# Performance work log

Measured on AMD Instinct MI355X. Metric: run time of the kernel, lower is better.

Reference implementation:

```python
import jax, jax.numpy as jnp
import numpy as np

B, H, S, D = 2, 16, 2048, 128
EPS = 1e-12  # F.normalize default eps
NEG = -1000000000.0


def setup_inputs() -> dict:
    key = jax.random.key(0)
    kq, kk, kv, km = jax.random.split(key, 4)
    q = jax.random.normal(kq, (B, H, S, D), dtype=jnp.float32)
    k = jax.random.normal(kk, (B, H, S, D), dtype=jnp.float32)
    v = jax.random.normal(kv, (B, H, S, D), dtype=jnp.float32)
    mask = jax.random.randint(km, (B, 1, 1, S), 0, 2).astype(jnp.int32)
    return {"q": q, "k": k, "v": v, "mask": mask}


def reference(q, k, v, mask):
    # L2-normalize k along dim=1 (the HEAD axis), matching F.normalize(k, p=2, dim=1)
    k_norm = k / jnp.maximum(jnp.linalg.norm(k, axis=1, keepdims=True), EPS)
    # attn scores: [B,H,S,S]
    attn = jnp.einsum('bhqd,bhkd->bhqk', q, k_norm)
    attn = jnp.where(mask == 0, NEG, attn)
    attn = jax.nn.softmax(attn, axis=-1)
    # dropout is identity in eval mode (deterministic reference)
    out = jnp.einsum('bhqk,bhkd->bhqd', attn, v)
    return (out, attn)
```

## Files before the change

kernel.cpp:

```cpp
#include <hip/hip_runtime.h>
#include <hip/hip_fp16.h>

#define BB 2
#define HH 16
#define SS 2048
#define DD 128
#define CH 64
#define NCH 32
#define QBLK 32
#define CSHIFT 14.0f

typedef __attribute__((ext_vector_type(8))) _Float16 f16x8;
typedef __attribute__((ext_vector_type(4))) _Float16 f16x4;
typedef __attribute__((ext_vector_type(4))) float    f32x4;

__device__ __forceinline__ void load_lds16(const void* g, void* l) {
  __builtin_amdgcn_global_load_lds(
      (const __attribute__((address_space(1))) void*)g,
      (__attribute__((address_space(3))) void*)l, 16, 0, 0);
}

__device__ __forceinline__ void block_barrier() {
  asm volatile("" ::: "memory");
  __builtin_amdgcn_s_barrier();
  asm volatile("" ::: "memory");
}

__global__ void knorm_f16(const float* __restrict__ k, _Float16* __restrict__ kh) {
  int t = blockIdx.x * 256 + threadIdx.x;
  int d = t & (DD - 1);
  int s = (t >> 7) & (SS - 1);
  int b = t >> 18;
  const float* kp = k + (size_t)b * HH * SS * DD + (size_t)s * DD + d;
  float vals[HH];
  float ss = 0.f;
  #pragma unroll
  for (int h = 0; h < HH; ++h) { float x = kp[(size_t)h * SS * DD]; vals[h] = x; ss += x * x; }
  float r = 1.0f / fmaxf(sqrtf(ss), 1e-12f);
  const int doff = (((d >> 3) ^ (s & 7)) << 3) + (d & 7);
  _Float16* op = kh + (size_t)b * HH * SS * DD + (size_t)s * DD + doff;
  #pragma unroll
  for (int h = 0; h < HH; ++h) op[(size_t)h * SS * DD] = (_Float16)(vals[h] * r);
}

__global__ void cvt_f16(const float* __restrict__ x, _Float16* __restrict__ y) {
  size_t i = ((size_t)blockIdx.x * 256 + threadIdx.x) * 8;
  float4 a = *(const float4*)(x + i);
  float4 b = *(const float4*)(x + i + 4);
  f16x8 r = { (_Float16)a.x, (_Float16)a.y, (_Float16)a.z, (_Float16)a.w,
              (_Float16)b.x, (_Float16)b.y, (_Float16)b.z, (_Float16)b.w };
  *(f16x8*)(y + i) = r;
}

__global__ void vtrans_f16(const float* __restrict__ v, _Float16* __restrict__ vt) {
  __shared__ float tile[32][33];
  int bh = blockIdx.z;
  int d0 = blockIdx.x * 32, s0 = blockIdx.y * 32;
  const float* vp = v + (size_t)bh * SS * DD;
  _Float16* tp = vt + (size_t)bh * SS * DD;
  int tx = threadIdx.x, ty = threadIdx.y;
  #pragma unroll
  for (int i = ty; i < 32; i += 8)
    tile[i][tx] = vp[(size_t)(s0 + i) * DD + d0 + tx];
  __syncthreads();
  #pragma unroll
  for (int i = ty; i < 32; i += 8) {
    const int key = s0 + tx, dd = d0 + i;
    tp[(size_t)(key >> 6) * (DD * CH) + (size_t)dd * CH
       + ((((key & 63) >> 3) ^ (dd & 7)) << 3) + (key & 7)] = (_Float16)tile[tx][i];
  }
}

__global__ __launch_bounds__(512, 4) void attn_fused(
    const _Float16* __restrict__ qh, const _Float16* __restrict__ kh,
    const _Float16* __restrict__ vth, const int* __restrict__ mask,
    float* __restrict__ out, float* __restrict__ attn)
{
  __shared__ _Float16 kbuf[2][CH * DD];
  __shared__ _Float16 vbuf[2][DD * CH];
  __shared__ _Float16 pbuf[2][QBLK * CH];
  __shared__ float redsum[2][16][5];

  const int wgid = blockIdx.x;
  const int xcd  = wgid & 7;
  const int idx  = wgid >> 3;
  const int bh   = (xcd << 2) | (idx >> 6);
  const int q0   = (idx & 63) * QBLK;
  const int b    = bh >> 4;

  const int tid  = threadIdx.x;
  const int lane = tid & 63;
  const int w    = tid >> 6;
  const int lo16 = lane & 15;
  const int g    = lane >> 4;
  const int qhf  = w >> 2;
  const int sub  = w & 3;

  const size_t hoff = (size_t)bh * SS * DD;
  const _Float16* Q = qh  + hoff + (size_t)q0 * DD;
  const _Float16* K = kh  + hoff;
  const _Float16* V = vth + hoff;
  const int* mrow = mask + b * SS;

  const int prow = qhf * 16 + lo16;

  f16x8 qf[4];
  #pragma unroll
  for (int c = 0; c < 4; ++c)
    qf[c] = *(const f16x8*)(Q + (size_t)prow * DD + c * 32 + g * 8);

  #pragma unroll
  for (int j = 0; j < 2; ++j) {
    const int slot = tid + j * 512;
    load_lds16(K + slot * 8, &kbuf[0][slot * 8]);
  }
  __syncthreads();

  f16x4 acc_h[NCH];
  f32x4 oacc[2] = { {0,0,0,0}, {0,0,0,0} };
  float ssum = 0.f;

  #pragma unroll
  for (int c = 0; c < NCH; ++c) {
    const _Float16* kb = kbuf[c & 1];

    if (c + 1 < NCH) {
      #pragma unroll
      for (int j = 0; j < 2; ++j) {
        const int slot = tid + j * 512;
        load_lds16(K + (size_t)(c + 1) * (CH * DD) + slot * 8,
                   &kbuf[(c + 1) & 1][slot * 8]);
      }
    }
    #pragma unroll
    for (int j = 0; j < 2; ++j) {
      const int slot = tid + j * 512;
      load_lds16(V + (size_t)c * (CH * DD) + slot * 8,
                 &vbuf[c & 1][slot * 8]);
    }

    {
      const int row = sub * 16 + lo16;
      f32x4 a = {0.f, 0.f, 0.f, 0.f};
      #pragma unroll
      for (int cc = 0; cc < 4; ++cc) {
        const int p = (cc * 4 + g) ^ (row & 7);
        f16x8 kf = *(const f16x8*)(kb + row * DD + p * 8);
        a = __builtin_amdgcn_mfma_f32_16x16x32_f16(kf, qf[cc], a, 0, 0, 0);
      }
      const int4 mv = *(const int4*)(mrow + c * CH + sub * 16 + g * 4);
      const float e0 = mv.x ? __expf(a[0] - CSHIFT) : 0.f;
      const float e1 = mv.y ? __expf(a[1] - CSHIFT) : 0.f;
      const float e2 = mv.z ? __expf(a[2] - CSHIFT) : 0.f;
      const float e3 = mv.w ? __expf(a[3] - CSHIFT) : 0.f;
      ssum += e0 + e1 + e2 + e3;
      f16x4 eh = { (_Float16)e0, (_Float16)e1, (_Float16)e2, (_Float16)e3 };
      acc_h[c] = eh;
      const int col = sub * 16 + g * 4;
      *(f16x4*)(&pbuf[c & 1][prow * CH + (((col >> 3) ^ (prow & 7)) << 3) + (col & 7)]) = eh;
    }

    if (c > 0) {
      const _Float16* vb = vbuf[(c - 1) & 1];
      const _Float16* pb = pbuf[(c - 1) & 1];
      #pragma unroll
      for (int t = 0; t < 2; ++t) {
        const int dcol = sub * 32 + t * 16 + lo16;
        #pragma unroll
        for (int ks = 0; ks < 2; ++ks) {
          const int pv_ = (ks * 4 + g) ^ (dcol & 7);
          f16x8 vf = *(const f16x8*)(vb + dcol * CH + pv_ * 8);
          f16x8 pf = *(const f16x8*)(pb + prow * CH + ((ks * 32 + g * 8) ^ ((prow & 7) << 3)));
          oacc[t] = __builtin_amdgcn_mfma_f32_16x16x32_f16(pf, vf, oacc[t], 0, 0, 0);
        }
      }
    }

    asm volatile("s_waitcnt lgkmcnt(0)" ::: "memory");
    asm volatile("s_waitcnt vmcnt(0)"  ::: "memory");
    block_barrier();
  }

  {
    const _Float16* vb = vbuf[(NCH - 1) & 1];
    const _Float16* pb = pbuf[(NCH - 1) & 1];
    #pragma unroll
    for (int t = 0; t < 2; ++t) {
      const int dcol = sub * 32 + t * 16 + lo16;
      #pragma unroll
      for (int ks = 0; ks < 2; ++ks) {
        const int pv_ = (ks * 4 + g) ^ (dcol & 7);
        f16x8 vf = *(const f16x8*)(vb + dcol * CH + pv_ * 8);
        f16x8 pf = *(const f16x8*)(pb + prow * CH + ((ks * 32 + g * 8) ^ ((prow & 7) << 3)));
        oacc[t] = __builtin_amdgcn_mfma_f32_16x16x32_f16(pf, vf, oacc[t], 0, 0, 0);
      }
    }
  }

  ssum += __shfl_xor(ssum, 16);
  ssum += __shfl_xor(ssum, 32);
  if (lane < 16) redsum[qhf][lane][sub] = ssum;
  __syncthreads();

  float denom = 0.f;
  #pragma unroll
  for (int j = 0; j < 4; ++j) denom += redsum[qhf][lo16][j];
  const float inv = 1.0f / denom;

  float* arow = attn + ((size_t)bh * SS + q0 + prow) * SS + sub * 16 + g * 4;
  #pragma unroll
  for (int c = 0; c < NCH; ++c) {
    f32x4 pst = { (float)acc_h[c][0] * inv, (float)acc_h[c][1] * inv,
                  (float)acc_h[c][2] * inv, (float)acc_h[c][3] * inv };
    *(f32x4*)(arow + c * CH) = pst;
  }

  float* O = out + hoff + (size_t)q0 * DD + sub * 32;
  #pragma unroll
  for (int i = 0; i < 4; ++i) {
    const int qr = g * 4 + i;
    float dq = 0.f;
    #pragma unroll
    for (int j = 0; j < 4; ++j) dq += redsum[qhf][qr][j];
    const float rdq = 1.0f / dq;
    #pragma unroll
    for (int t = 0; t < 2; ++t)
      O[(size_t)(qhf * 16 + qr) * DD + t * 16 + lo16] = oacc[t][i] * rdq;
  }
}

extern "C" void kernel_launch(void* const* d_in, const int* in_sizes, int n_in,
                              void* d_out, int out_size, void* d_ws, size_t ws_size,
                              hipStream_t stream) {
  const float* q    = (const float*)d_in[0];
  const float* k    = (const float*)d_in[1];
  const float* v    = (const float*)d_in[2];
  const int*   mask = (const int*)d_in[3];

  const size_t N = (size_t)BB * HH * SS * DD;
  float* out  = (float*)d_out;
  float* attn = out + N;

  _Float16* qh  = (_Float16*)d_ws;
  _Float16* kh  = qh + N;
  _Float16* vth = kh + N;

  cvt_f16  <<<N / 8 / 256, 256, 0, stream>>>(q, qh);
  knorm_f16<<<(BB * SS * DD) / 256, 256, 0, stream>>>(k, kh);
  vtrans_f16<<<dim3(DD / 32, SS / 32, BB * HH), dim3(32, 8), 0, stream>>>(v, vth);

  attn_fused<<<2048, 512, 0, stream>>>(qh, kh, vth, mask, out, attn);
}
```

Measured before the change: 313.1 us.

## Double query block per workgroup and triple-buffer K/V prefetch two chunks ahead

Each workgroup now handles 64 query rows with 1024 threads (16 waves), so every K/V chunk loaded into LDS is shared by twice as many rows and the grid is halved. K and V use triple buffering: K is prefetched two chunks ahead and V one chunk ahead, and the per-iteration wait becomes vmcnt(1), which lets the most recent K load stay in flight across the barrier. The larger workgroup raises LDS use, and the 1024-thread launch bounds may cap registers per thread, which could cause spills given the large per-thread array of f16 score fragments.

Result: no change. 316.4 us (+1.0%).

```diff
diff --git a/kernel.cpp b/kernel.cpp
--- a/kernel.cpp
+++ b/kernel.cpp
@@ -7,7 +7,7 @@
 #define DD 128
 #define CH 64
 #define NCH 32
-#define QBLK 32
+#define QBLK 64
 #define CSHIFT 14.0f
 
 typedef __attribute__((ext_vector_type(8))) _Float16 f16x8;
@@ -71,21 +71,21 @@
   }
 }
 
-__global__ __launch_bounds__(512, 4) void attn_fused(
+__global__ __launch_bounds__(1024, 4) void attn_fused(
     const _Float16* __restrict__ qh, const _Float16* __restrict__ kh,
     const _Float16* __restrict__ vth, const int* __restrict__ mask,
     float* __restrict__ out, float* __restrict__ attn)
 {
-  __shared__ _Float16 kbuf[2][CH * DD];
-  __shared__ _Float16 vbuf[2][DD * CH];
+  __shared__ _Float16 kbuf[3][CH * DD];
+  __shared__ _Float16 vbuf[3][DD * CH];
   __shared__ _Float16 pbuf[2][QBLK * CH];
-  __shared__ float redsum[2][16][5];
+  __shared__ float redsum[4][16][5];
 
   const int wgid = blockIdx.x;
   const int xcd  = wgid & 7;
   const int idx  = wgid >> 3;
-  const int bh   = (xcd << 2) | (idx >> 6);
-  const int q0   = (idx & 63) * QBLK;
+  const int bh   = (xcd << 2) | (idx >> 5);
+  const int q0   = (idx & 31) * QBLK;
   const int b    = bh >> 4;
 
   const int tid  = threadIdx.x;
@@ -93,7 +93,7 @@
   const int w    = tid >> 6;
   const int lo16 = lane & 15;
   const int g    = lane >> 4;
-  const int qhf  = w >> 2;
+  const int qq   = w >> 2;
   const int sub  = w & 3;
 
   const size_t hoff = (size_t)bh * SS * DD;
@@ -102,18 +102,16 @@
   const _Float16* V = vth + hoff;
   const int* mrow = mask + b * SS;
 
-  const int prow = qhf * 16 + lo16;
+  const int prow = qq * 16 + lo16;
 
   f16x8 qf[4];
   #pragma unroll
   for (int c = 0; c < 4; ++c)
     qf[c] = *(const f16x8*)(Q + (size_t)prow * DD + c * 32 + g * 8);
 
-  #pragma unroll
-  for (int j = 0; j < 2; ++j) {
-    const int slot = tid + j * 512;
-    load_lds16(K + slot * 8, &kbuf[0][slot * 8]);
-  }
+  load_lds16(V + tid * 8, &vbuf[0][tid * 8]);
+  load_lds16(K + tid * 8, &kbuf[0][tid * 8]);
+  load_lds16(K + (size_t)(CH * DD) + tid * 8, &kbuf[1][tid * 8]);
   __syncthreads();
 
   f16x4 acc_h[NCH];
@@ -122,22 +120,14 @@
 
   #pragma unroll
   for (int c = 0; c < NCH; ++c) {
-    const _Float16* kb = kbuf[c & 1];
-
-    if (c + 1 < NCH) {
-      #pragma unroll
-      for (int j = 0; j < 2; ++j) {
-        const int slot = tid + j * 512;
-        load_lds16(K + (size_t)(c + 1) * (CH * DD) + slot * 8,
-                   &kbuf[(c + 1) & 1][slot * 8]);
-      }
-    }
-    #pragma unroll
-    for (int j = 0; j < 2; ++j) {
-      const int slot = tid + j * 512;
-      load_lds16(V + (size_t)c * (CH * DD) + slot * 8,
-                 &vbuf[c & 1][slot * 8]);
-    }
+    const _Float16* kb = kbuf[c % 3];
+
+    if (c + 1 < NCH)
+      load_lds16(V + (size_t)(c + 1) * (CH * DD) + tid * 8,
+                 &vbuf[(c + 1) % 3][tid * 8]);
+    if (c + 2 < NCH)
+      load_lds16(K + (size_t)(c + 2) * (CH * DD) + tid * 8,
+                 &kbuf[(c + 2) % 3][tid * 8]);
 
     {
       const int row = sub * 16 + lo16;
@@ -161,7 +151,7 @@
     }
 
     if (c > 0) {
-      const _Float16* vb = vbuf[(c - 1) & 1];
+      const _Float16* vb = vbuf[(c - 1) % 3];
       const _Float16* pb = pbuf[(c - 1) & 1];
       #pragma unroll
       for (int t = 0; t < 2; ++t) {
@@ -177,12 +167,16 @@
     }
 
     asm volatile("s_waitcnt lgkmcnt(0)" ::: "memory");
-    asm volatile("s_waitcnt vmcnt(0)"  ::: "memory");
+    if (c + 2 < NCH) {
+      asm volatile("s_waitcnt vmcnt(1)" ::: "memory");
+    } else {
+      asm volatile("s_waitcnt vmcnt(0)" ::: "memory");
+    }
     block_barrier();
   }
 
   {
-    const _Float16* vb = vbuf[(NCH - 1) & 1];
+    const _Float16* vb = vbuf[(NCH - 1) % 3];
     const _Float16* pb = pbuf[(NCH - 1) & 1];
     #pragma unroll
     for (int t = 0; t < 2; ++t) {
@@ -199,12 +193,12 @@
 
   ssum += __shfl_xor(ssum, 16);
   ssum += __shfl_xor(ssum, 32);
-  if (lane < 16) redsum[qhf][lane][sub] = ssum;
+  if (lane < 16) redsum[qq][lane][sub] = ssum;
   __syncthreads();
 
   float denom = 0.f;
   #pragma unroll
-  for (int j = 0; j < 4; ++j) denom += redsum[qhf][lo16][j];
+  for (int j = 0; j < 4; ++j) denom += redsum[qq][lo16][j];
   const float inv = 1.0f / denom;
 
   float* arow = attn + ((size_t)bh * SS + q0 + prow) * SS + sub * 16 + g * 4;
@@ -221,11 +215,11 @@
     const int qr = g * 4 + i;
     float dq = 0.f;
     #pragma unroll
-    for (int j = 0; j < 4; ++j) dq += redsum[qhf][qr][j];
+    for (int j = 0; j < 4; ++j) dq += redsum[qq][qr][j];
     const float rdq = 1.0f / dq;
     #pragma unroll
     for (int t = 0; t < 2; ++t)
-      O[(size_t)(qhf * 16 + qr) * DD + t * 16 + lo16] = oacc[t][i] * rdq;
+      O[(size_t)(qq * 16 + qr) * DD + t * 16 + lo16] = oacc[t][i] * rdq;
   }
 }
 
@@ -249,5 +243,5 @@
   knorm_f16<<<(BB * SS * DD) / 256, 256, 0, stream>>>(k, kh);
   vtrans_f16<<<dim3(DD / 32, SS / 32, BB * HH), dim3(32, 8), 0, stream>>>(v, vth);
 
-  attn_fused<<<2048, 512, 0, stream>>>(qh, kh, vth, mask, out, attn);
-}
+  attn_fused<<<1024, 1024, 0, stream>>>(qh, kh, vth, mask, out, attn);
+}
```
